# Optimization experiments

Hardware: AMD Instinct MI355X
Metric: run time of the kernel (lower is better)

Reference implementation:

```python
import jax, jax.numpy as jnp
import numpy as np

B, DAYS, N, E = 2, 8, 10000, 80000
C_IN, C_OUT, H = 32, 32, 4
NEG_SLOPE = 0.2


def setup_inputs() -> dict:
    key = jax.random.key(0)
    ks = jax.random.split(key, 7)
    x = jax.random.randint(ks[0], (B, DAYS, N), 0, N)
    adjacency = jax.random.randint(ks[1], (2, E), 0, N)
    embedding = jax.random.normal(ks[2], (N, C_IN), dtype=jnp.float32)
    # GATConv linear: in_channels -> heads*out_channels
    W = jax.random.normal(ks[3], (C_IN, H * C_OUT), dtype=jnp.float32) / np.sqrt(C_IN)
    att_src = jax.random.normal(ks[4], (H, C_OUT), dtype=jnp.float32) / np.sqrt(C_OUT)
    att_dst = jax.random.normal(ks[5], (H, C_OUT), dtype=jnp.float32) / np.sqrt(C_OUT)
    bias = jnp.zeros((H * C_OUT,), dtype=jnp.float32)
    return {"x": x, "adjacency": adjacency, "embedding": embedding,
            "W": W, "att_src": att_src, "att_dst": att_dst, "bias": bias}


def _gat_forward(feat, src, dst, W, att_src, att_dst, bias):
    # feat: [G, N, C_IN]; same edge list shared across the G graphs
    G = feat.shape[0]
    xh = (feat @ W).reshape(G, N, H, C_OUT)              # [G,N,H,C]
    a_src = jnp.einsum('gnhc,hc->gnh', xh, att_src)       # [G,N,H]
    a_dst = jnp.einsum('gnhc,hc->gnh', xh, att_dst)
    alpha = a_src[:, src] + a_dst[:, dst]                 # [G,Et,H]
    alpha = jnp.where(alpha >= 0, alpha, NEG_SLOPE * alpha)

    def per_graph(al, msgs):
        # segment softmax over incoming edges of each dst node
        m = jax.ops.segment_max(al, dst, num_segments=N)  # [N,H]
        e = jnp.exp(al - m[dst])                          # [Et,H]
        s = jax.ops.segment_sum(e, dst, num_segments=N)
        w = e / (s[dst] + 1e-16)
        out = jax.ops.segment_sum(w[..., None] * msgs, dst, num_segments=N)
        return out                                        # [N,H,C]

    out = jax.vmap(per_graph)(alpha, xh[:, src])          # [G,N,H,C]
    return out.reshape(G, N, H * C_OUT) + bias


def reference(x, adjacency, embedding, W, att_src, att_dst, bias):
    Bd, Dd = x.shape[0], x.shape[1]
    feat = embedding[x].reshape(-1, N, C_IN)              # [G,N,C_IN]
    # GATConv default add_self_loops=True
    loops = jnp.arange(N, dtype=adjacency.dtype)
    src = jnp.concatenate([adjacency[0], loops])
    dst = jnp.concatenate([adjacency[1], loops])
    out = _gat_forward(feat, src, dst, W, att_src, att_dst, bias)
    return out.reshape(Bd, Dd, -1)
```

## Files before the change

kernel.cpp:

```cpp
#include <hip/hip_runtime.h>
#include <hip/hip_bf16.h>
#include <math.h>

#define C_IN 32
#define H 4
#define C_OUT 32
#define HC (H * C_OUT)
#define NEG_SLOPE 0.2f
#define CSR_STRIDE 64

typedef float v2f __attribute__((ext_vector_type(2)));

#define RPB 16
__global__ __launch_bounds__(256) void build_kernel(
        const int* __restrict__ adj, int E, int N,
        int* __restrict__ deg, int* __restrict__ csr,
        const float* __restrict__ emb, const float* __restrict__ W,
        const float* __restrict__ att_src, const float* __restrict__ att_dst,
        __hip_bfloat16* __restrict__ T, float* __restrict__ ta_src,
        float* __restrict__ ta_dst, int tblocks) {
    if ((int)blockIdx.x >= tblocks) {
        int e = (blockIdx.x - tblocks) * 256 + threadIdx.x;
        int Et = E + N;
        if (e < Et) {
            int s = (e < E) ? adj[e] : (e - E);
            int d = (e < E) ? adj[E + e] : (e - E);
            int pos = atomicAdd(&deg[d], 1);
            if (pos < CSR_STRIDE) csr[(d << 6) + pos] = s;
        }
        return;
    }
    int t = threadIdx.x;
    int sub = t >> 7;
    int tc = t & 127;
    int h = tc >> 5, c = tc & 31;
    int base = blockIdx.x * RPB;
    int nmax = (N - base < RPB) ? (N - base) : RPB;

    float wcol[C_IN];
#pragma unroll
    for (int k = 0; k < C_IN; k++) wcol[k] = W[k * HC + tc];
    float as = att_src[h * C_OUT + c];
    float adw = att_dst[h * C_OUT + c];

    for (int it = sub; it < nmax; it += 2) {
        int r = __builtin_amdgcn_readfirstlane(base + it);
        const float* ep = emb + (size_t)r * C_IN;
        float acc = 0.f;
#pragma unroll
        for (int k = 0; k < C_IN; k++) acc += ep[k] * wcol[k];
        T[(size_t)r * HC + tc] = __float2bfloat16(acc);
        float ps = acc * as, pd = acc * adw;
#pragma unroll
        for (int o = 16; o; o >>= 1) {
            ps += __shfl_xor(ps, o, 32);
            pd += __shfl_xor(pd, o, 32);
        }
        if (c == 0) {
            ta_src[r * H + h] = ps;
            ta_dst[r * H + h] = pd;
        }
    }
}

__global__ __launch_bounds__(256) void agg_kernel(
        const int* __restrict__ deg, const int* __restrict__ csr,
        const int* __restrict__ x, const unsigned int* __restrict__ Tu,
        const float* __restrict__ ta_src, const float* __restrict__ ta_dst,
        const float* __restrict__ bias, float* __restrict__ out, int N, int G) {
    int wid = threadIdx.x >> 6;
    int lane = threadIdx.x & 63;
    int n = blockIdx.x;
    int h2 = lane >> 4;
    int g0 = wid * 4;
    if (g0 >= G) return;

    int dg = deg[n];
    if (dg > CSR_STRIDE) dg = CSR_STRIDE;
    const int* cb = csr + (n << 6);

    float ad[4];
    v2f acc[4];
    float dsum[4];
#pragma unroll
    for (int j = 0; j < 4; j++) {
        int gj = g0 + j;
        int xgn = __builtin_amdgcn_readfirstlane(x[(size_t)gj * N + n]);
        ad[j] = ta_dst[xgn * H + h2];
        acc[j] = (v2f){0.f, 0.f};
        dsum[j] = 0.f;
    }

#pragma unroll 2
    for (int e = 0; e < dg; e++) {
        int s = __builtin_amdgcn_readfirstlane(cb[e]);
        size_t sbase = (size_t)g0 * N + s;
#pragma unroll
        for (int j = 0; j < 4; j++) {
            int xs = __builtin_amdgcn_readfirstlane(x[sbase + (size_t)j * N]);
            float a = ta_src[xs * H + h2] + ad[j];
            a = fmaxf(a, NEG_SLOPE * a);
            float w = __expf(a);
            unsigned int u = Tu[(xs << 6) + lane];
            v2f t = {__uint_as_float(u << 16),
                     __uint_as_float(u & 0xffff0000u)};
            acc[j] += (v2f){w, w} * t;
            dsum[j] += w;
        }
    }

    float2 b2 = *(const float2*)(bias + lane * 2);
    size_t obase = (size_t)n * HC + lane * 2;
#pragma unroll
    for (int j = 0; j < 4; j++) {
        int gj = g0 + j;
        float inv = __builtin_amdgcn_rcpf(dsum[j] + 1e-16f);
        float2 o2;
        o2.x = acc[j].x * inv + b2.x;
        o2.y = acc[j].y * inv + b2.y;
        *(float2*)(out + obase + (size_t)gj * N * HC) = o2;
    }
}

extern "C" void kernel_launch(void* const* d_in, const int* in_sizes, int n_in,
                              void* d_out, int out_size, void* d_ws, size_t ws_size,
                              hipStream_t stream) {
    const int*   x       = (const int*)d_in[0];
    const int*   adj     = (const int*)d_in[1];
    const float* emb     = (const float*)d_in[2];
    const float* W       = (const float*)d_in[3];
    const float* att_src = (const float*)d_in[4];
    const float* att_dst = (const float*)d_in[5];
    const float* bias    = (const float*)d_in[6];
    float* out = (float*)d_out;

    const int N  = in_sizes[2] / C_IN;
    const int GN = in_sizes[0];
    const int G  = GN / N;
    const int E  = in_sizes[1] / 2;
    const int Et = E + N;

    char* ws = (char*)d_ws;
    size_t o = 0;
    auto carve = [&](size_t bytes) -> void* {
        void* p = ws + o;
        o = (o + bytes + 255) & ~(size_t)255;
        return p;
    };
    __hip_bfloat16* T = (__hip_bfloat16*)carve((size_t)N * HC * sizeof(__hip_bfloat16));
    float* ta_src  = (float*)carve((size_t)N * H * sizeof(float));
    float* ta_dst  = (float*)carve((size_t)N * H * sizeof(float));
    int*   deg     = (int*)carve((size_t)N * sizeof(int));
    int*   csr     = (int*)carve((size_t)N * CSR_STRIDE * sizeof(int));

    hipMemsetAsync(deg, 0, (size_t)N * sizeof(int), stream);

    int tblocks = (N + RPB - 1) / RPB;
    int fblocks = (Et + 255) / 256;
    build_kernel<<<tblocks + fblocks, 256, 0, stream>>>(
        adj, E, N, deg, csr, emb, W, att_src, att_dst, T, ta_src, ta_dst, tblocks);

    agg_kernel<<<N, 256, 0, stream>>>(deg, csr, x,
                                      (const unsigned int*)T, ta_src, ta_dst,
                                      bias, out, N, G);
}
```

Baseline: 163.2 us.

## Precompute edge attention weights cooperatively in LDS before aggregation loop

```diff
diff --git a/kernel.cpp b/kernel.cpp
--- a/kernel.cpp
+++ b/kernel.cpp
@@ -68,44 +68,61 @@
         const int* __restrict__ x, const unsigned int* __restrict__ Tu,
         const float* __restrict__ ta_src, const float* __restrict__ ta_dst,
         const float* __restrict__ bias, float* __restrict__ out, int N, int G) {
-    int wid = threadIdx.x >> 6;
-    int lane = threadIdx.x & 63;
+    __shared__ float w_lds[16][CSR_STRIDE][4];
+    __shared__ int   xs_lds[16][CSR_STRIDE];
+    __shared__ float ds_lds[16][4];
+
+    int t = threadIdx.x;
     int n = blockIdx.x;
-    int h2 = lane >> 4;
-    int g0 = wid * 4;
-    if (g0 >= G) return;
-
     int dg = deg[n];
     if (dg > CSR_STRIDE) dg = CSR_STRIDE;
     const int* cb = csr + (n << 6);
 
-    float ad[4];
+    {
+        int g = t >> 4;
+        int es = (t >> 2) & 3;
+        int h = t & 3;
+        int xgn = x[(size_t)g * N + n];
+        float adv = ta_dst[xgn * H + h];
+        float dpart = 0.f;
+        for (int c0 = 0; c0 < dg; c0 += 4) {
+            int e = c0 + es;
+            if (e < dg) {
+                int s = cb[e];
+                int xs = x[(size_t)g * N + s];
+                float a = ta_src[xs * H + h] + adv;
+                a = fmaxf(a, NEG_SLOPE * a);
+                float w = __expf(a);
+                w_lds[g][e][h] = w;
+                dpart += w;
+                if (h == 0) xs_lds[g][e] = xs;
+            }
+        }
+        dpart += __shfl_xor(dpart, 4, 64);
+        dpart += __shfl_xor(dpart, 8, 64);
+        if (es == 0) ds_lds[g][h] = dpart;
+    }
+    __syncthreads();
+
+    int wid = t >> 6;
+    int lane = t & 63;
+    int h2 = lane >> 4;
+    int g0 = wid * 4;
+
     v2f acc[4];
-    float dsum[4];
 #pragma unroll
-    for (int j = 0; j < 4; j++) {
-        int gj = g0 + j;
-        int xgn = __builtin_amdgcn_readfirstlane(x[(size_t)gj * N + n]);
-        ad[j] = ta_dst[xgn * H + h2];
-        acc[j] = (v2f){0.f, 0.f};
-        dsum[j] = 0.f;
-    }
+    for (int j = 0; j < 4; j++) acc[j] = (v2f){0.f, 0.f};
 
 #pragma unroll 2
     for (int e = 0; e < dg; e++) {
-        int s = __builtin_amdgcn_readfirstlane(cb[e]);
-        size_t sbase = (size_t)g0 * N + s;
 #pragma unroll
         for (int j = 0; j < 4; j++) {
-            int xs = __builtin_amdgcn_readfirstlane(x[sbase + (size_t)j * N]);
-            float a = ta_src[xs * H + h2] + ad[j];
-            a = fmaxf(a, NEG_SLOPE * a);
-            float w = __expf(a);
+            int xs = __builtin_amdgcn_readfirstlane(xs_lds[g0 + j][e]);
+            float w = w_lds[g0 + j][e][h2];
             unsigned int u = Tu[(xs << 6) + lane];
-            v2f t = {__uint_as_float(u << 16),
-                     __uint_as_float(u & 0xffff0000u)};
-            acc[j] += (v2f){w, w} * t;
-            dsum[j] += w;
+            v2f tr = {__uint_as_float(u << 16),
+                      __uint_as_float(u & 0xffff0000u)};
+            acc[j] += (v2f){w, w} * tr;
         }
     }
 
@@ -114,7 +131,7 @@
 #pragma unroll
     for (int j = 0; j < 4; j++) {
         int gj = g0 + j;
-        float inv = __builtin_amdgcn_rcpf(dsum[j] + 1e-16f);
+        float inv = __builtin_amdgcn_rcpf(ds_lds[gj][h2] + 1e-16f);
         float2 o2;
         o2.x = acc[j].x * inv + b2.x;
         o2.y = acc[j].y * inv + b2.y;
```

Result: faster. 157.6 us (-3.4%).
